# Kernel tuning notes

Measured on AMD Instinct MI355X. Metric: run time of the kernel, lower is better.

The kernel has to match this reference:

```python
import jax, jax.numpy as jnp
import numpy as np

N = 100000   # n_nodes (= ninput, identity features)
E = 1600000  # edges per adjacency (avg degree 16)
H = 128      # nhid
EPS = 1e-12


def setup_inputs() -> dict:
    key = jax.random.key(0)
    ks = jax.random.split(key, 24)
    inp = {
        'adj1_rows': jax.random.randint(ks[0], (E,), 0, N),
        'adj1_cols': jax.random.randint(ks[1], (E,), 0, N),
        'adj1_vals': jax.random.uniform(ks[2], (E,), jnp.float32) / 16.0,
        'adj2_rows': jax.random.randint(ks[3], (E,), 0, N),
        'adj2_cols': jax.random.randint(ks[4], (E,), 0, N),
        'adj2_vals': jax.random.uniform(ks[5], (E,), jnp.float32) / 16.0,
    }
    s = 1.0 / np.sqrt(H)
    inp['w1'] = jax.random.uniform(ks[6], (N, H), jnp.float32, -s, s)
    for i in range(2, 10):
        inp[f'w{i}'] = jax.random.uniform(ks[5 + i], (H, H), jnp.float32, -s, s)
    s2 = 1.0 / np.sqrt(2 * H)
    inp['m1'] = jax.random.uniform(ks[15], (H, 2 * H), jnp.float32, -s, s)
    inp['b1'] = jnp.zeros((2 * H,), jnp.float32)
    inp['m2'] = jax.random.uniform(ks[16], (2 * H, 2 * H), jnp.float32, -s2, s2)
    inp['b2'] = jnp.zeros((2 * H,), jnp.float32)
    inp['m3'] = jax.random.uniform(ks[17], (2 * H, 1), jnp.float32, -s2, s2)
    inp['b3'] = jnp.zeros((1,), jnp.float32)
    return inp


def _spmm(rows, cols, vals, x):
    # sparse [N,N] @ dense [N,H] via gather + segment_sum
    return jax.ops.segment_sum(vals[:, None] * x[cols], rows, num_segments=N)


def _l2norm(x):
    # F.normalize(x, p=2, dim=1)
    n = jnp.sqrt(jnp.sum(x * x, axis=1, keepdims=True))
    return x / jnp.maximum(n, EPS)


def _mlp(x, m1, b1, m2, b2, m3, b3):
    # dropout inactive (eval mode) for deterministic reference
    h = jax.nn.relu(x @ m1 + b1)
    h = jax.nn.relu(h @ m2 + b2)
    return h @ m3 + b3  # [N,1]


def _branch(rows, cols, vals, w1, ws, mlp_params):
    x = jax.nn.relu(_spmm(rows, cols, vals, w1))
    x = _l2norm(x)
    score = _mlp(x, *mlp_params)
    for i, w in enumerate(ws):
        x = jax.nn.relu(_spmm(rows, cols, vals, x @ w))
        if i < len(ws) - 1:  # last layer (gc9) is relu only, no normalize
            x = _l2norm(x)
        score = score + _mlp(x, *mlp_params)
    return score


def reference(adj1_rows, adj1_cols, adj1_vals, adj2_rows, adj2_cols, adj2_vals,
              w1, w2, w3, w4, w5, w6, w7, w8, w9,
              m1, b1, m2, b2, m3, b3):
    ws = [w2, w3, w4, w5, w6, w7, w8, w9]
    mlp_params = (m1, b1, m2, b2, m3, b3)
    score1 = _branch(adj1_rows, adj1_cols, adj1_vals, w1, ws, mlp_params)
    score2 = _branch(adj2_rows, adj2_cols, adj2_vals, w1, ws, mlp_params)
    return score1 * score2  # [N,1]
```

## Files before the change

kernel.cpp:

```cpp
#include <hip/hip_runtime.h>
#include <hip/hip_fp16.h>

#define NN 100000
#define NE 1600000
#define HD 128
#define HD2 256

typedef unsigned int u32;
typedef unsigned short u16;
typedef _Float16 half8 __attribute__((ext_vector_type(8)));
typedef float floatx4 __attribute__((ext_vector_type(4)));

static inline int cdiv(int a, int b){ return (a + b - 1) / b; }

__device__ __forceinline__ u32 split_pack(float v){
  __half h;
  if(fabsf(v) < 6.103515625e-05f) h = __ushort_as_half((u16)0);
  else h = __float2half_rn(v);
  float hf = __half2float(h);
  __half l = __float2half_rn((v - hf) * 4096.0f);
  return (u32)__half_as_ushort(h) | ((u32)__half_as_ushort(l) << 16);
}

__global__ void k_zero_int(int* __restrict__ p, int n){
  int i = blockIdx.x * 256 + threadIdx.x;
  if(i < n) p[i] = 0;
}

__global__ void k_zero_f(float* __restrict__ p, int n){
  int i = blockIdx.x * 256 + threadIdx.x;
  if(i < n) p[i] = 0.f;
}

__global__ void k_hist2(const int* __restrict__ r0, const int* __restrict__ r1,
                        int* __restrict__ cnt){
  int e = blockIdx.x * 256 + threadIdx.x;
  if(e < NE){
    const int* rows = blockIdx.y ? r1 : r0;
    atomicAdd(&cnt[blockIdx.y * NN + rows[e]], 1);
  }
}

__global__ void k_scan1b(const int* __restrict__ cnt, int* __restrict__ p0,
                         int* __restrict__ p1, int* __restrict__ sums, int n){
  __shared__ int sh[256];
  int z = blockIdx.y;
  const int* c = cnt + z * n;
  int* part = z ? p1 : p0;
  int* sm = sums + z * 128;
  int tid = threadIdx.x;
  int base = blockIdx.x * 1024 + tid * 4;
  int v0 = (base + 0 < n) ? c[base + 0] : 0;
  int v1 = (base + 1 < n) ? c[base + 1] : 0;
  int v2 = (base + 2 < n) ? c[base + 2] : 0;
  int v3 = (base + 3 < n) ? c[base + 3] : 0;
  int s = v0 + v1 + v2 + v3;
  sh[tid] = s;
  __syncthreads();
  for(int d = 1; d < 256; d <<= 1){
    int t = (tid >= d) ? sh[tid - d] : 0;
    __syncthreads();
    sh[tid] += t;
    __syncthreads();
  }
  int excl = sh[tid] - s;
  if(tid == 255) sm[blockIdx.x] = sh[255];
  if(base + 0 < n) part[base + 0] = excl;
  if(base + 1 < n) part[base + 1] = excl + v0;
  if(base + 2 < n) part[base + 2] = excl + v0 + v1;
  if(base + 3 < n) part[base + 3] = excl + v0 + v1 + v2;
}

__global__ void k_scan2b(int* __restrict__ sums, int nb){
  __shared__ int sh[128];
  int* s = sums + blockIdx.x * 128;
  int tid = threadIdx.x;
  int v = (tid < nb) ? s[tid] : 0;
  sh[tid] = v;
  __syncthreads();
  for(int d = 1; d < 128; d <<= 1){
    int t = (tid >= d) ? sh[tid - d] : 0;
    __syncthreads();
    sh[tid] += t;
    __syncthreads();
  }
  if(tid < nb) s[tid] = sh[tid] - v;
}

__global__ void k_scan3b(int* __restrict__ r0, int* __restrict__ r1,
                         int* __restrict__ cursor, const int* __restrict__ sums, int n){
  int z = blockIdx.y;
  int* rowptr = z ? r1 : r0;
  int* cur = cursor + z * n;
  int off = sums[z * 128 + blockIdx.x];
  int tid = threadIdx.x;
  int base = blockIdx.x * 1024 + tid * 4;
  #pragma unroll
  for(int j = 0; j < 4; j++){
    int idx = base + j;
    if(idx < n){ int r = rowptr[idx] + off; rowptr[idx] = r; cur[idx] = r; }
  }
  if(blockIdx.x == 0 && tid == 0) rowptr[n] = NE;
}

__global__ void k_scatter2(const int* __restrict__ r0, const int* __restrict__ c0,
                           const float* __restrict__ v0,
                           const int* __restrict__ r1, const int* __restrict__ c1,
                           const float* __restrict__ v1,
                           int* __restrict__ cursor,
                           uint2* __restrict__ e0, uint2* __restrict__ e1){
  int e = blockIdx.x * 256 + threadIdx.x;
  if(e < NE){
    int z = blockIdx.y;
    const int* rows = z ? r1 : r0;
    const int* cols = z ? c1 : c0;
    const float* vals = z ? v1 : v0;
    int* cur = cursor + z * NN;
    uint2* ecv = z ? e1 : e0;
    int r = rows[e];
    int pp = atomicAdd(&cur[r], 1);
    ecv[pp] = make_uint2((u32)cols[e], __float_as_uint(vals[e]));
  }
}

__global__ void k_splitw(const float* __restrict__ W, u32* __restrict__ out,
                         int K, int N, int total){
  int idx = blockIdx.x * 256 + threadIdx.x;
  if(idx < total){
    int n = idx / K, k = idx - n * K;
    out[idx] = split_pack(W[(size_t)k * N + n]);
  }
}

template<bool NORM>
__global__ void k_spmm(const int* __restrict__ rowptr, const uint2* __restrict__ ecv,
                       const float* __restrict__ X, u32* __restrict__ outpk){
  int node = (blockIdx.x << 2) + (threadIdx.x >> 6);
  int lane = threadIdx.x & 63;
  if(node >= NN) return;
  int s = rowptr[node], e = rowptr[node + 1];
  float ax = 0.f, ay = 0.f, bx = 0.f, by = 0.f;
  int i = s;
  for(; i + 15 < e; i += 16){
    uint2 ee[16]; float2 xx[16];
    #pragma unroll
    for(int j = 0; j < 16; j++) ee[j] = ecv[i + j];
    #pragma unroll
    for(int j = 0; j < 16; j++) xx[j] = *(const float2*)(X + (size_t)ee[j].x * HD + lane * 2);
    #pragma unroll
    for(int j = 0; j < 16; j += 4){
      ax += __uint_as_float(ee[j].y)   * xx[j].x   + __uint_as_float(ee[j+1].y) * xx[j+1].x;
      ay += __uint_as_float(ee[j].y)   * xx[j].y   + __uint_as_float(ee[j+1].y) * xx[j+1].y;
      bx += __uint_as_float(ee[j+2].y) * xx[j+2].x + __uint_as_float(ee[j+3].y) * xx[j+3].x;
      by += __uint_as_float(ee[j+2].y) * xx[j+2].y + __uint_as_float(ee[j+3].y) * xx[j+3].y;
    }
  }
  for(; i + 3 < e; i += 4){
    uint2 f0 = ecv[i], f1 = ecv[i+1], f2 = ecv[i+2], f3 = ecv[i+3];
    float2 x0 = *(const float2*)(X + (size_t)f0.x * HD + lane * 2);
    float2 x1 = *(const float2*)(X + (size_t)f1.x * HD + lane * 2);
    float2 x2 = *(const float2*)(X + (size_t)f2.x * HD + lane * 2);
    float2 x3 = *(const float2*)(X + (size_t)f3.x * HD + lane * 2);
    ax += __uint_as_float(f0.y) * x0.x + __uint_as_float(f1.y) * x1.x;
    ay += __uint_as_float(f0.y) * x0.y + __uint_as_float(f1.y) * x1.y;
    bx += __uint_as_float(f2.y) * x2.x + __uint_as_float(f3.y) * x3.x;
    by += __uint_as_float(f2.y) * x2.y + __uint_as_float(f3.y) * x3.y;
  }
  for(; i < e; i++){
    uint2 f0 = ecv[i];
    float2 xv = *(const float2*)(X + (size_t)f0.x * HD + lane * 2);
    ax += __uint_as_float(f0.y) * xv.x;
    ay += __uint_as_float(f0.y) * xv.y;
  }
  ax += bx; ay += by;
  ax = fmaxf(ax, 0.f);
  ay = fmaxf(ay, 0.f);
  if(NORM){
    float ss = ax * ax + ay * ay;
    #pragma unroll
    for(int o = 32; o >= 1; o >>= 1) ss += __shfl_xor(ss, o, 64);
    float scale = 1.f / fmaxf(sqrtf(ss), 1e-12f);
    ax *= scale; ay *= scale;
  }
  *(uint2*)(outpk + (size_t)node * HD + lane * 2) = make_uint2(split_pack(ax), split_pack(ay));
}

template<int MODE>
__launch_bounds__(256, 2)
__global__ void k_mfma_gemm(const u32* __restrict__ Apk, const u32* __restrict__ Btpk,
                            const u32* __restrict__ Bt1pk,
                            const float* __restrict__ bias, float* __restrict__ Yout,
                            u32* __restrict__ Hout, const float* __restrict__ m3,
                            float* __restrict__ score, int M, int K, int N){
  __shared__ u16 As_h[128 * 40], As_l[128 * 40];
  __shared__ u16 Bs_h[128 * 40], Bs_l[128 * 40];
  const int tid = threadIdx.x;
  const int lane = tid & 63, wid = tid >> 6;
  const int lm = lane & 15, lg = lane >> 4;
  const int mq = (wid & 1) * 64, nq = (wid >> 1) * 64;
  const int m0 = blockIdx.x * 128;
  int n0 = blockIdx.y * 128;
  const u32* Bt = Btpk;
  bool m0path = true;
  if(MODE == 3){
    m0path = (blockIdx.y == 0);
    if(m0path){ n0 = 0; }
    else      { n0 = (blockIdx.y - 1) * 128; Bt = Bt1pk; }
  }

  floatx4 accA[4][4], accB[4][4];
  #pragma unroll
  for(int i = 0; i < 4; i++)
    #pragma unroll
    for(int j = 0; j < 4; j++){
      accA[i][j] = (floatx4){0.f, 0.f, 0.f, 0.f};
      accB[i][j] = (floatx4){0.f, 0.f, 0.f, 0.f};
    }

  for(int k0 = 0; k0 < K; k0 += 32){
    uint4 av[4], bv[4];
    #pragma unroll
    for(int j = 0; j < 4; j++){
      int li = tid + j * 256;
      int row = li >> 3, kc = (li & 7) * 4;
      int ar = m0 + row; if(ar >= M) ar = M - 1;
      av[j] = *(const uint4*)(Apk + (size_t)ar * K + k0 + kc);
      bv[j] = *(const uint4*)(Bt + (size_t)(n0 + row) * K + k0 + kc);
    }
    if(k0) __syncthreads();
    #pragma unroll
    for(int j = 0; j < 4; j++){
      int li = tid + j * 256;
      int row = li >> 3, kc = (li & 7) * 4;
      int base = row * 40 + kc;
      ushort4 h, l;
      h.x = (u16)(av[j].x & 0xffff); l.x = (u16)(av[j].x >> 16);
      h.y = (u16)(av[j].y & 0xffff); l.y = (u16)(av[j].y >> 16);
      h.z = (u16)(av[j].z & 0xffff); l.z = (u16)(av[j].z >> 16);
      h.w = (u16)(av[j].w & 0xffff); l.w = (u16)(av[j].w >> 16);
      *(ushort4*)&As_h[base] = h;
      *(ushort4*)&As_l[base] = l;
      h.x = (u16)(bv[j].x & 0xffff); l.x = (u16)(bv[j].x >> 16);
      h.y = (u16)(bv[j].y & 0xffff); l.y = (u16)(bv[j].y >> 16);
      h.z = (u16)(bv[j].z & 0xffff); l.z = (u16)(bv[j].z >> 16);
      h.w = (u16)(bv[j].w & 0xffff); l.w = (u16)(bv[j].w >> 16);
      *(ushort4*)&Bs_h[base] = h;
      *(ushort4*)&Bs_l[base] = l;
    }
    __syncthreads();

    half8 fa_h[4], fa_l[4], fb_h[4], fb_l[4];
    #pragma unroll
    for(int s = 0; s < 4; s++){
      int ra = (mq + s * 16 + lm) * 40 + lg * 8;
      fa_h[s] = *(const half8*)&As_h[ra];
      fa_l[s] = *(const half8*)&As_l[ra];
      int rb = (nq + s * 16 + lm) * 40 + lg * 8;
      fb_h[s] = *(const half8*)&Bs_h[rb];
      fb_l[s] = *(const half8*)&Bs_l[rb];
    }
    #pragma unroll
    for(int i = 0; i < 4; i++)
      #pragma unroll
      for(int j = 0; j < 4; j++){
        accA[i][j] = __builtin_amdgcn_mfma_f32_16x16x32_f16(fa_h[i], fb_h[j], accA[i][j], 0, 0, 0);
        accB[i][j] = __builtin_amdgcn_mfma_f32_16x16x32_f16(fa_h[i], fb_l[j], accB[i][j], 0, 0, 0);
        accB[i][j] = __builtin_amdgcn_mfma_f32_16x16x32_f16(fa_l[i], fb_h[j], accB[i][j], 0, 0, 0);
      }
  }

  const float inv4096 = 1.f / 4096.f;
  if(MODE == 0 || (MODE == 3 && m0path)){
    int ldy = (MODE == 3) ? HD : N;
    #pragma unroll
    for(int i = 0; i < 4; i++)
      #pragma unroll
      for(int r = 0; r < 4; r++){
        int m = m0 + mq + i * 16 + lg * 4 + r;
        if(m < M){
          #pragma unroll
          for(int j = 0; j < 4; j++){
            int c = n0 + nq + j * 16 + lm;
            Yout[(size_t)m * ldy + c] = accA[i][j][r] + accB[i][j][r] * inv4096;
          }
        }
      }
  } else if(MODE == 1 || MODE == 3){
    int ldh = (MODE == 3) ? HD2 : N;
    #pragma unroll
    for(int i = 0; i < 4; i++)
      #pragma unroll
      for(int r = 0; r < 4; r++){
        int m = m0 + mq + i * 16 + lg * 4 + r;
        if(m < M){
          #pragma unroll
          for(int j = 0; j < 4; j++){
            int c = n0 + nq + j * 16 + lm;
            float v = fmaxf(accA[i][j][r] + accB[i][j][r] * inv4096 + bias[c], 0.f);
            Hout[(size_t)m * ldh + c] = split_pack(v);
          }
        }
      }
  } else {
    #pragma unroll
    for(int i = 0; i < 4; i++)
      #pragma unroll
      for(int r = 0; r < 4; r++){
        float s = 0.f;
        #pragma unroll
        for(int j = 0; j < 4; j++){
          int c = n0 + nq + j * 16 + lm;
          float v = fmaxf(accA[i][j][r] + accB[i][j][r] * inv4096 + bias[c], 0.f);
          s = fmaf(v, m3[c], s);
        }
        s += __shfl_xor(s, 1, 64);
        s += __shfl_xor(s, 2, 64);
        s += __shfl_xor(s, 4, 64);
        s += __shfl_xor(s, 8, 64);
        int m = m0 + mq + i * 16 + lg * 4 + r;
        if(lm == 0 && m < M) atomicAdd(&score[m], s);
      }
  }
}

__global__ void k_final(const float* __restrict__ sc, const float* __restrict__ b3,
                        float* __restrict__ out){
  int i = blockIdx.x * 256 + threadIdx.x;
  if(i < NN){
    float b = 9.f * b3[0];
    out[i] = (sc[i] + b) * (sc[NN + i] + b);
  }
}

extern "C" void kernel_launch(void* const* d_in, const int* in_sizes, int n_in,
                              void* d_out, int out_size, void* d_ws, size_t ws_size,
                              hipStream_t stream){
  const int*   a1r = (const int*)d_in[0];
  const int*   a1c = (const int*)d_in[1];
  const float* a1v = (const float*)d_in[2];
  const int*   a2r = (const int*)d_in[3];
  const int*   a2c = (const int*)d_in[4];
  const float* a2v = (const float*)d_in[5];
  const float* w1  = (const float*)d_in[6];
  const float* w[8];
  for(int i = 0; i < 8; i++) w[i] = (const float*)d_in[7 + i];
  const float* m1 = (const float*)d_in[15];
  const float* b1 = (const float*)d_in[16];
  const float* m2 = (const float*)d_in[17];
  const float* b2 = (const float*)d_in[18];
  const float* m3 = (const float*)d_in[19];
  const float* b3 = (const float*)d_in[20];
  float* out = (float*)d_out;

  char* base = (char*)d_ws;
  size_t off = 0;
  auto alloc = [&](size_t bytes) -> char* {
    char* r = base + off;
    off += (bytes + 255) & ~(size_t)255;
    return r;
  };
  int*   c1ptr = (int*)  alloc((size_t)(NN + 1) * 4);
  int*   c2ptr = (int*)  alloc((size_t)(NN + 1) * 4);
  uint2* ecv1  = (uint2*)alloc((size_t)NE * 8);
  uint2* ecv2  = (uint2*)alloc((size_t)NE * 8);
  int*   cursor= (int*)  alloc((size_t)2 * NN * 4);
  int*   sums  = (int*)  alloc(1024);
  float* sc    = (float*)alloc((size_t)2 * NN * 4);
  u32*   wtpk[8];
  for(int i = 0; i < 8; i++) wtpk[i] = (u32*)alloc((size_t)HD * HD * 4);
  u32*   m1tpk = (u32*)alloc((size_t)HD2 * HD * 4);
  u32*   m2tpk = (u32*)alloc((size_t)HD2 * HD2 * 4);
  u32*   xpk   = (u32*)alloc((size_t)NN * HD * 4);
  u32*   h1pk  = (u32*)alloc((size_t)NN * HD2 * 4);
  size_t need_ded = off + (((size_t)NN * HD * 4 + 255) & ~(size_t)255);
  bool ded_y = (ws_size >= need_ded);
  float* y = ded_y ? (float*)alloc((size_t)NN * HD * 4) : (float*)h1pk;

  hipLaunchKernelGGL(k_zero_int, dim3(cdiv(2 * NN, 256)), dim3(256), 0, stream, cursor, 2 * NN);
  hipLaunchKernelGGL(k_hist2, dim3(cdiv(NE, 256), 2), dim3(256), 0, stream, a1r, a2r, cursor);
  const int SCAN_BLOCKS = cdiv(NN, 1024);
  hipLaunchKernelGGL(k_scan1b, dim3(SCAN_BLOCKS, 2), dim3(256), 0, stream, cursor, c1ptr, c2ptr, sums, NN);
  hipLaunchKernelGGL(k_scan2b, dim3(2), dim3(128), 0, stream, sums, SCAN_BLOCKS);
  hipLaunchKernelGGL(k_scan3b, dim3(SCAN_BLOCKS, 2), dim3(256), 0, stream, c1ptr, c2ptr, cursor, sums, NN);
  hipLaunchKernelGGL(k_scatter2, dim3(cdiv(NE, 256), 2), dim3(256), 0, stream,
                     a1r, a1c, a1v, a2r, a2c, a2v, cursor, ecv1, ecv2);

  auto splitw = [&](const float* W, u32* o, int K, int N){
    int total = K * N;
    hipLaunchKernelGGL(k_splitw, dim3(cdiv(total, 256)), dim3(256), 0, stream, W, o, K, N, total);
  };
  for(int i = 0; i < 8; i++) splitw(w[i], wtpk[i], HD, HD);
  splitw(m1, m1tpk, HD, HD2);
  splitw(m2, m2tpk, HD2, HD2);
  hipLaunchKernelGGL(k_zero_f, dim3(cdiv(2 * NN, 256)), dim3(256), 0, stream, sc, 2 * NN);

  const int GX = cdiv(NN, 128);
  auto mode1 = [&](){
    hipLaunchKernelGGL((k_mfma_gemm<1>), dim3(GX, 2), dim3(256), 0, stream,
                       xpk, m1tpk, (const u32*)nullptr, b1, (float*)nullptr, h1pk,
                       (const float*)nullptr, (float*)nullptr, NN, HD, HD2);
  };
  auto mode2 = [&](float* score){
    hipLaunchKernelGGL((k_mfma_gemm<2>), dim3(GX, 2), dim3(256), 0, stream,
                       h1pk, m2tpk, (const u32*)nullptr, b2, (float*)nullptr, (u32*)nullptr,
                       m3, score, NN, HD2, HD2);
  };
  auto gemm0 = [&](int i){
    hipLaunchKernelGGL((k_mfma_gemm<0>), dim3(GX, 1), dim3(256), 0, stream,
                       xpk, wtpk[i], (const u32*)nullptr, (const float*)nullptr, y, (u32*)nullptr,
                       (const float*)nullptr, (float*)nullptr, NN, HD, HD);
  };
  auto fused01 = [&](int i){
    hipLaunchKernelGGL((k_mfma_gemm<3>), dim3(GX, 3), dim3(256), 0, stream,
                       xpk, wtpk[i], m1tpk, b1, y, h1pk,
                       (const float*)nullptr, (float*)nullptr, NN, HD, 0);
  };

  for(int b = 0; b < 2; b++){
    const int* rp = b ? c2ptr : c1ptr;
    const uint2* ecv = b ? ecv2 : ecv1;
    float* score = sc + (size_t)b * NN;
    hipLaunchKernelGGL((k_spmm<true>), dim3(cdiv(NN, 4)), dim3(256), 0, stream,
                       rp, ecv, w1, xpk);
    if(ded_y){
      for(int i = 0; i < 8; i++){
        fused01(i);
        mode2(score);
        if(i < 7)
          hipLaunchKernelGGL((k_spmm<true>),  dim3(cdiv(NN, 4)), dim3(256), 0, stream,
                             rp, ecv, y, xpk);
        else
          hipLaunchKernelGGL((k_spmm<false>), dim3(cdiv(NN, 4)), dim3(256), 0, stream,
                             rp, ecv, y, xpk);
      }
      mode1();
      mode2(score);
    } else {
      mode1();
      mode2(score);
      for(int i = 0; i < 8; i++){
        gemm0(i);
        if(i < 7)
          hipLaunchKernelGGL((k_spmm<true>),  dim3(cdiv(NN, 4)), dim3(256), 0, stream,
                             rp, ecv, y, xpk);
        else
          hipLaunchKernelGGL((k_spmm<false>), dim3(cdiv(NN, 4)), dim3(256), 0, stream,
                             rp, ecv, y, xpk);
        mode1();
        mode2(score);
      }
    }
  }

  hipLaunchKernelGGL(k_final, dim3(cdiv(NN, 256)), dim3(256), 0, stream, sc, b3, out);
}
```

Measured before the change: 4.715 ms.

## Split packed hi/lo fp16 planes and use direct global-to-LDS loads in MFMA GEMM

Activation and weight buffers change from interleaved u32 hi/lo packs to separate fp16 high and low planes. The GEMM now stages the full K=128 chunk of A straight into LDS with global_load_lds, using an XOR swizzle, in place of register unpacking. B fragments are read directly from global memory with no shared-memory staging. This is meant to cut the unpack ALU work and the LDS write traffic, at the cost of a larger LDS footprint (64KB per block), which may lower occupancy, and of uncoalesced, repeated global reads for B.

```diff
diff --git a/kernel.cpp b/kernel.cpp
--- a/kernel.cpp
+++ b/kernel.cpp
@@ -20,6 +20,11 @@
   float hf = __half2float(h);
   __half l = __float2half_rn((v - hf) * 4096.0f);
   return (u32)__half_as_ushort(h) | ((u32)__half_as_ushort(l) << 16);
+}
+
+__device__ __forceinline__ void gl_lds16(const u16* g, u16* l){
+  __builtin_amdgcn_global_load_lds((const __attribute__((address_space(1))) u32*)g,
+                                   (__attribute__((address_space(3))) u32*)l, 16, 0, 0);
 }
 
 __global__ void k_zero_int(int* __restrict__ p, int n){
@@ -123,18 +128,21 @@
   }
 }
 
-__global__ void k_splitw(const float* __restrict__ W, u32* __restrict__ out,
-                         int K, int N, int total){
+__global__ void k_splitw(const float* __restrict__ W, u16* __restrict__ oh,
+                         u16* __restrict__ ol, int K, int N, int total){
   int idx = blockIdx.x * 256 + threadIdx.x;
   if(idx < total){
     int n = idx / K, k = idx - n * K;
-    out[idx] = split_pack(W[(size_t)k * N + n]);
+    u32 p = split_pack(W[(size_t)k * N + n]);
+    oh[idx] = (u16)(p & 0xffffu);
+    ol[idx] = (u16)(p >> 16);
   }
 }
 
 template<bool NORM>
 __global__ void k_spmm(const int* __restrict__ rowptr, const uint2* __restrict__ ecv,
-                       const float* __restrict__ X, u32* __restrict__ outpk){
+                       const float* __restrict__ X, u16* __restrict__ Xh,
+                       u16* __restrict__ Xl){
   int node = (blockIdx.x << 2) + (threadIdx.x >> 6);
   int lane = threadIdx.x & 63;
   if(node >= NN) return;
@@ -182,30 +190,34 @@
     float scale = 1.f / fmaxf(sqrtf(ss), 1e-12f);
     ax *= scale; ay *= scale;
   }
-  *(uint2*)(outpk + (size_t)node * HD + lane * 2) = make_uint2(split_pack(ax), split_pack(ay));
+  u32 p0 = split_pack(ax), p1 = split_pack(ay);
+  *(u32*)(Xh + (size_t)node * HD + lane * 2) = (p0 & 0xffffu) | ((p1 & 0xffffu) << 16);
+  *(u32*)(Xl + (size_t)node * HD + lane * 2) = (p0 >> 16) | (p1 & 0xffff0000u);
 }
 
 template<int MODE>
 __launch_bounds__(256, 2)
-__global__ void k_mfma_gemm(const u32* __restrict__ Apk, const u32* __restrict__ Btpk,
-                            const u32* __restrict__ Bt1pk,
+__global__ void k_mfma_gemm(const u16* __restrict__ Ah, const u16* __restrict__ Al,
+                            const u16* __restrict__ Bh, const u16* __restrict__ Bl,
+                            const u16* __restrict__ B1h, const u16* __restrict__ B1l,
                             const float* __restrict__ bias, float* __restrict__ Yout,
-                            u32* __restrict__ Hout, const float* __restrict__ m3,
-                            float* __restrict__ score, int M, int K, int N){
-  __shared__ u16 As_h[128 * 40], As_l[128 * 40];
-  __shared__ u16 Bs_h[128 * 40], Bs_l[128 * 40];
+                            u16* __restrict__ Hh, u16* __restrict__ Hl,
+                            const float* __restrict__ m3, float* __restrict__ score,
+                            int M, int K, int N){
+  __shared__ u16 As_h[128 * 128];
+  __shared__ u16 As_l[128 * 128];
   const int tid = threadIdx.x;
   const int lane = tid & 63, wid = tid >> 6;
   const int lm = lane & 15, lg = lane >> 4;
   const int mq = (wid & 1) * 64, nq = (wid >> 1) * 64;
   const int m0 = blockIdx.x * 128;
   int n0 = blockIdx.y * 128;
-  const u32* Bt = Btpk;
+  const u16* Bth = Bh; const u16* Btl = Bl;
   bool m0path = true;
   if(MODE == 3){
     m0path = (blockIdx.y == 0);
     if(m0path){ n0 = 0; }
-    else      { n0 = (blockIdx.y - 1) * 128; Bt = Bt1pk; }
+    else      { n0 = (blockIdx.y - 1) * 128; Bth = B1h; Btl = B1l; }
   }
 
   floatx4 accA[4][4], accB[4][4];
@@ -217,56 +229,43 @@
       accB[i][j] = (floatx4){0.f, 0.f, 0.f, 0.f};
     }
 
-  for(int k0 = 0; k0 < K; k0 += 32){
-    uint4 av[4], bv[4];
-    #pragma unroll
-    for(int j = 0; j < 4; j++){
+  for(int kc = 0; kc < K; kc += 128){
+    if(kc) __syncthreads();
+    #pragma unroll
+    for(int j = 0; j < 8; j++){
       int li = tid + j * 256;
-      int row = li >> 3, kc = (li & 7) * 4;
+      int row = li >> 4, slot = li & 15;
+      int g = slot ^ (row & 15);
       int ar = m0 + row; if(ar >= M) ar = M - 1;
-      av[j] = *(const uint4*)(Apk + (size_t)ar * K + k0 + kc);
-      bv[j] = *(const uint4*)(Bt + (size_t)(n0 + row) * K + k0 + kc);
-    }
-    if(k0) __syncthreads();
-    #pragma unroll
-    for(int j = 0; j < 4; j++){
-      int li = tid + j * 256;
-      int row = li >> 3, kc = (li & 7) * 4;
-      int base = row * 40 + kc;
-      ushort4 h, l;
-      h.x = (u16)(av[j].x & 0xffff); l.x = (u16)(av[j].x >> 16);
-      h.y = (u16)(av[j].y & 0xffff); l.y = (u16)(av[j].y >> 16);
-      h.z = (u16)(av[j].z & 0xffff); l.z = (u16)(av[j].z >> 16);
-      h.w = (u16)(av[j].w & 0xffff); l.w = (u16)(av[j].w >> 16);
-      *(ushort4*)&As_h[base] = h;
-      *(ushort4*)&As_l[base] = l;
-      h.x = (u16)(bv[j].x & 0xffff); l.x = (u16)(bv[j].x >> 16);
-      h.y = (u16)(bv[j].y & 0xffff); l.y = (u16)(bv[j].y >> 16);
-      h.z = (u16)(bv[j].z & 0xffff); l.z = (u16)(bv[j].z >> 16);
-      h.w = (u16)(bv[j].w & 0xffff); l.w = (u16)(bv[j].w >> 16);
-      *(ushort4*)&Bs_h[base] = h;
-      *(ushort4*)&Bs_l[base] = l;
+      size_t so = (size_t)ar * K + kc + g * 8;
+      gl_lds16(Ah + so, &As_h[li * 8]);
+      gl_lds16(Al + so, &As_l[li * 8]);
     }
     __syncthreads();
-
-    half8 fa_h[4], fa_l[4], fb_h[4], fb_l[4];
-    #pragma unroll
-    for(int s = 0; s < 4; s++){
-      int ra = (mq + s * 16 + lm) * 40 + lg * 8;
-      fa_h[s] = *(const half8*)&As_h[ra];
-      fa_l[s] = *(const half8*)&As_l[ra];
-      int rb = (nq + s * 16 + lm) * 40 + lg * 8;
-      fb_h[s] = *(const half8*)&Bs_h[rb];
-      fb_l[s] = *(const half8*)&Bs_l[rb];
+    #pragma unroll
+    for(int ks = 0; ks < 4; ks++){
+      half8 fa_h[4], fa_l[4], fb_h[4], fb_l[4];
+      #pragma unroll
+      for(int s = 0; s < 4; s++){
+        int col = n0 + nq + s * 16 + lm;
+        size_t bo = (size_t)col * K + kc + ks * 32 + lg * 8;
+        fb_h[s] = *(const half8*)(Bth + bo);
+        fb_l[s] = *(const half8*)(Btl + bo);
+        int rowt = mq + s * 16 + lm;
+        int sl = (ks * 4 + lg) ^ (rowt & 15);
+        int ai = rowt * 128 + sl * 8;
+        fa_h[s] = *(const half8*)&As_h[ai];
+        fa_l[s] = *(const half8*)&As_l[ai];
+      }
+      #pragma unroll
+      for(int i = 0; i < 4; i++)
+        #pragma unroll
+        for(int j = 0; j < 4; j++){
+          accA[i][j] = __builtin_amdgcn_mfma_f32_16x16x32_f16(fa_h[i], fb_h[j], accA[i][j], 0, 0, 0);
+          accB[i][j] = __builtin_amdgcn_mfma_f32_16x16x32_f16(fa_h[i], fb_l[j], accB[i][j], 0, 0, 0);
+          accB[i][j] = __builtin_amdgcn_mfma_f32_16x16x32_f16(fa_l[i], fb_h[j], accB[i][j], 0, 0, 0);
+        }
     }
-    #pragma unroll
-    for(int i = 0; i < 4; i++)
-      #pragma unroll
-      for(int j = 0; j < 4; j++){
-        accA[i][j] = __builtin_amdgcn_mfma_f32_16x16x32_f16(fa_h[i], fb_h[j], accA[i][j], 0, 0, 0);
-        accB[i][j] = __builtin_amdgcn_mfma_f32_16x16x32_f16(fa_h[i], fb_l[j], accB[i][j], 0, 0, 0);
-        accB[i][j] = __builtin_amdgcn_mfma_f32_16x16x32_f16(fa_l[i], fb_h[j], accB[i][j], 0, 0, 0);
-      }
   }
 
   const float inv4096 = 1.f / 4096.f;
@@ -286,7 +285,6 @@
         }
       }
   } else if(MODE == 1 || MODE == 3){
-    int ldh = (MODE == 3) ? HD2 : N;
     #pragma unroll
     for(int i = 0; i < 4; i++)
       #pragma unroll
@@ -297,7 +295,9 @@
           for(int j = 0; j < 4; j++){
             int c = n0 + nq + j * 16 + lm;
             float v = fmaxf(accA[i][j][r] + accB[i][j][r] * inv4096 + bias[c], 0.f);
-            Hout[(size_t)m * ldh + c] = split_pack(v);
+            u32 p = split_pack(v);
+            Hh[(size_t)m * HD2 + c] = (u16)(p & 0xffffu);
+            Hl[(size_t)m * HD2 + c] = (u16)(p >> 16);
           }
         }
       }
@@ -366,15 +366,22 @@
   int*   cursor= (int*)  alloc((size_t)2 * NN * 4);
   int*   sums  = (int*)  alloc(1024);
   float* sc    = (float*)alloc((size_t)2 * NN * 4);
-  u32*   wtpk[8];
-  for(int i = 0; i < 8; i++) wtpk[i] = (u32*)alloc((size_t)HD * HD * 4);
-  u32*   m1tpk = (u32*)alloc((size_t)HD2 * HD * 4);
-  u32*   m2tpk = (u32*)alloc((size_t)HD2 * HD2 * 4);
-  u32*   xpk   = (u32*)alloc((size_t)NN * HD * 4);
-  u32*   h1pk  = (u32*)alloc((size_t)NN * HD2 * 4);
+  u16*   wth[8]; u16* wtl[8];
+  for(int i = 0; i < 8; i++){
+    wth[i] = (u16*)alloc((size_t)HD * HD * 2);
+    wtl[i] = (u16*)alloc((size_t)HD * HD * 2);
+  }
+  u16*   m1h = (u16*)alloc((size_t)HD2 * HD * 2);
+  u16*   m1l = (u16*)alloc((size_t)HD2 * HD * 2);
+  u16*   m2h = (u16*)alloc((size_t)HD2 * HD2 * 2);
+  u16*   m2l = (u16*)alloc((size_t)HD2 * HD2 * 2);
+  u16*   Xh  = (u16*)alloc((size_t)NN * HD * 2);
+  u16*   Xl  = (u16*)alloc((size_t)NN * HD * 2);
+  u16*   H1h = (u16*)alloc((size_t)NN * HD2 * 2);
+  u16*   H1l = (u16*)alloc((size_t)NN * HD2 * 2);
   size_t need_ded = off + (((size_t)NN * HD * 4 + 255) & ~(size_t)255);
   bool ded_y = (ws_size >= need_ded);
-  float* y = ded_y ? (float*)alloc((size_t)NN * HD * 4) : (float*)h1pk;
+  float* y = ded_y ? (float*)alloc((size_t)NN * HD * 4) : (float*)H1h;
 
   hipLaunchKernelGGL(k_zero_int, dim3(cdiv(2 * NN, 256)), dim3(256), 0, stream, cursor, 2 * NN);
   hipLaunchKernelGGL(k_hist2, dim3(cdiv(NE, 256), 2), dim3(256), 0, stream, a1r, a2r, cursor);
@@ -385,34 +392,38 @@
   hipLaunchKernelGGL(k_scatter2, dim3(cdiv(NE, 256), 2), dim3(256), 0, stream,
                      a1r, a1c, a1v, a2r, a2c, a2v, cursor, ecv1, ecv2);
 
-  auto splitw = [&](const float* W, u32* o, int K, int N){
+  auto splitw = [&](const float* W, u16* oh, u16* ol, int K, int N){
     int total = K * N;
-    hipLaunchKernelGGL(k_splitw, dim3(cdiv(total, 256)), dim3(256), 0, stream, W, o, K, N, total);
-  };
-  for(int i = 0; i < 8; i++) splitw(w[i], wtpk[i], HD, HD);
-  splitw(m1, m1tpk, HD, HD2);
-  splitw(m2, m2tpk, HD2, HD2);
+    hipLaunchKernelGGL(k_splitw, dim3(cdiv(total, 256)), dim3(256), 0, stream, W, oh, ol, K, N, total);
+  };
+  for(int i = 0; i < 8; i++) splitw(w[i], wth[i], wtl[i], HD, HD);
+  splitw(m1, m1h, m1l, HD, HD2);
+  splitw(m2, m2h, m2l, HD2, HD2);
   hipLaunchKernelGGL(k_zero_f, dim3(cdiv(2 * NN, 256)), dim3(256), 0, stream, sc, 2 * NN);
 
   const int GX = cdiv(NN, 128);
   auto mode1 = [&](){
     hipLaunchKernelGGL((k_mfma_gemm<1>), dim3(GX, 2), dim3(256), 0, stream,
-                       xpk, m1tpk, (const u32*)nullptr, b1, (float*)nullptr, h1pk,
+                       Xh, Xl, m1h, m1l, (const u16*)nullptr, (const u16*)nullptr,
+                       b1, (float*)nullptr, H1h, H1l,
                        (const float*)nullptr, (float*)nullptr, NN, HD, HD2);
   };
   auto mode2 = [&](float* score){
     hipLaunchKernelGGL((k_mfma_gemm<2>), dim3(GX, 2), dim3(256), 0, stream,
-                       h1pk, m2tpk, (const u32*)nullptr, b2, (float*)nullptr, (u32*)nullptr,
+                       H1h, H1l, m2h, m2l, (const u16*)nullptr, (const u16*)nullptr,
+                       b2, (float*)nullptr, (u16*)nullptr, (u16*)nullptr,
                        m3, score, NN, HD2, HD2);
   };
   auto gemm0 = [&](int i){
     hipLaunchKernelGGL((k_mfma_gemm<0>), dim3(GX, 1), dim3(256), 0, stream,
-                       xpk, wtpk[i], (const u32*)nullptr, (const float*)nullptr, y, (u32*)nullptr,
+                       Xh, Xl, wth[i], wtl[i], (const u16*)nullptr, (const u16*)nullptr,
+                       (const float*)nullptr, y, (u16*)nullptr, (u16*)nullptr,
                        (const float*)nullptr, (float*)nullptr, NN, HD, HD);
   };
   auto fused01 = [&](int i){
     hipLaunchKernelGGL((k_mfma_gemm<3>), dim3(GX, 3), dim3(256), 0, stream,
-                       xpk, wtpk[i], m1tpk, b1, y, h1pk,
+                       Xh, Xl, wth[i], wtl[i], m1h, m1l,
+                       b1, y, H1h, H1l,
                        (const float*)nullptr, (float*)nullptr, NN, HD, 0);
   };
 
@@ -421,17 +432,17 @@
     const uint2* ecv = b ? ecv2 : ecv1;
     float* score = sc + (size_t)b * NN;
     hipLaunchKernelGGL((k_spmm<true>), dim3(cdiv(NN, 4)), dim3(256), 0, stream,
-                       rp, ecv, w1, xpk);
+                       rp, ecv, w1, Xh, Xl);
     if(ded_y){
       for(int i = 0; i < 8; i++){
         fused01(i);
         mode2(score);
         if(i < 7)
           hipLaunchKernelGGL((k_spmm<true>),  dim3(cdiv(NN, 4)), dim3(256), 0, stream,
-                             rp, ecv, y, xpk);
+                             rp, ecv, y, Xh, Xl);
         else
           hipLaunchKernelGGL((k_spmm<false>), dim3(cdiv(NN, 4)), dim3(256), 0, stream,
-                             rp, ecv, y, xpk);
+                             rp, ecv, y, Xh, Xl);
       }
       mode1();
       mode2(score);
@@ -442,10 +453,10 @@
         gemm0(i);
         if(i < 7)
           hipLaunchKernelGGL((k_spmm<true>),  dim3(cdiv(NN, 4)), dim3(256), 0, stream,
-                             rp, ecv, y, xpk);
+                             rp, ecv, y, Xh, Xl);
         else
           hipLaunchKernelGGL((k_spmm<false>), dim3(cdiv(NN, 4)), dim3(256), 0, stream,
-                             rp, ecv, y, xpk);
+                             rp, ecv, y, Xh, Xl);
         mode1();
         mode2(score);
       }
```

Result: slower. 7.598 ms (+61.2%).

## Replace atomic COO-to-CSR scatter with two-pass bucketed binning scatter

Applied to the files above, without the earlier changes.

The single-pass scatter, which did one global atomicAdd per edge into random rows, is replaced by two passes. The first pass bins each 4096-edge chunk in LDS by coarse row bucket (196 rows per bucket) and writes the chunk out in contiguous runs. The second pass places each bucket's edges into their rows using LDS atomics. This targets global atomic contention and scattered uncoalesced writes during CSR construction, at the cost of an extra round trip of edge data through a temporary buffer held in h1pk scratch. The CSR build is a one-time setup step next to many SpMM and GEMM layers, so the effect on total time may be small.

```diff
diff --git a/kernel.cpp b/kernel.cpp
--- a/kernel.cpp
+++ b/kernel.cpp
@@ -5,6 +5,10 @@
 #define NE 1600000
 #define HD 128
 #define HD2 256
+
+#define NBK 512
+#define RPB 196
+#define CH  4096
 
 typedef unsigned int u32;
 typedef unsigned short u16;
@@ -103,23 +107,113 @@
   if(blockIdx.x == 0 && tid == 0) rowptr[n] = NE;
 }
 
-__global__ void k_scatter2(const int* __restrict__ r0, const int* __restrict__ c0,
-                           const float* __restrict__ v0,
-                           const int* __restrict__ r1, const int* __restrict__ c1,
-                           const float* __restrict__ v1,
-                           int* __restrict__ cursor,
-                           uint2* __restrict__ e0, uint2* __restrict__ e1){
-  int e = blockIdx.x * 256 + threadIdx.x;
-  if(e < NE){
-    int z = blockIdx.y;
-    const int* rows = z ? r1 : r0;
-    const int* cols = z ? c1 : c0;
-    const float* vals = z ? v1 : v0;
-    int* cur = cursor + z * NN;
-    uint2* ecv = z ? e1 : e0;
-    int r = rows[e];
-    int pp = atomicAdd(&cur[r], 1);
-    ecv[pp] = make_uint2((u32)cols[e], __float_as_uint(vals[e]));
+__global__ void k_init_bcur(const int* __restrict__ c1ptr, const int* __restrict__ c2ptr,
+                            int* __restrict__ cursor){
+  int b = blockIdx.x * 256 + threadIdx.x;
+  int z = blockIdx.y;
+  if(b < NBK){
+    const int* rp = z ? c2ptr : c1ptr;
+    int r = b * RPB; if(r > NN) r = NN;
+    cursor[z * NN + b] = rp[r];
+  }
+}
+
+__global__ void k_binscatter(const int* __restrict__ r0a, const int* __restrict__ c0a,
+                             const float* __restrict__ v0a,
+                             const int* __restrict__ r1a, const int* __restrict__ c1a,
+                             const float* __restrict__ v1a,
+                             int* __restrict__ bcur,
+                             u32* __restrict__ sr0, uint2* __restrict__ sv0,
+                             u32* __restrict__ sr1, uint2* __restrict__ sv1){
+  __shared__ int cnt[NBK];
+  __shared__ int bstart[NBK];
+  __shared__ int gbase[NBK];
+  __shared__ int sh[256];
+  __shared__ u32 srow[CH];
+  __shared__ uint2 scvs[CH];
+  int z = blockIdx.y;
+  const int* rows = z ? r1a : r0a;
+  const int* cols = z ? c1a : c0a;
+  const float* vals = z ? v1a : v0a;
+  int* cur = bcur + z * NN;
+  u32* osr = z ? sr1 : sr0;
+  uint2* osv = z ? sv1 : sv0;
+  int t = threadIdx.x;
+  for(int i = t; i < NBK; i += 256) cnt[i] = 0;
+  __syncthreads();
+  int e0 = blockIdx.x * CH;
+  int total = NE - e0; if(total > CH) total = CH;
+  int r_[16], c_[16], b_[16], k_[16]; float v_[16];
+  #pragma unroll
+  for(int k = 0; k < 16; k++){
+    int e = e0 + t + k * 256;
+    b_[k] = -1;
+    if(e < NE){
+      r_[k] = rows[e]; c_[k] = cols[e]; v_[k] = vals[e];
+      b_[k] = r_[k] / RPB;
+      k_[k] = atomicAdd(&cnt[b_[k]], 1);
+    }
+  }
+  __syncthreads();
+  int v0 = cnt[2 * t], v1 = cnt[2 * t + 1];
+  int s2 = v0 + v1;
+  sh[t] = s2;
+  __syncthreads();
+  for(int d = 1; d < 256; d <<= 1){
+    int tv = (t >= d) ? sh[t - d] : 0;
+    __syncthreads();
+    sh[t] += tv;
+    __syncthreads();
+  }
+  int excl = sh[t] - s2;
+  bstart[2 * t] = excl;
+  bstart[2 * t + 1] = excl + v0;
+  __syncthreads();
+  #pragma unroll
+  for(int k = 0; k < 16; k++){
+    if(b_[k] >= 0){
+      int slot = bstart[b_[k]] + k_[k];
+      srow[slot] = (u32)r_[k];
+      scvs[slot] = make_uint2((u32)c_[k], __float_as_uint(v_[k]));
+    }
+  }
+  for(int b = t; b < NBK; b += 256){
+    int c = cnt[b];
+    if(c > 0) gbase[b] = atomicAdd(&cur[b], c);
+  }
+  __syncthreads();
+  for(int i = t; i < total; i += 256){
+    u32 r = srow[i];
+    int b = (int)r / RPB;
+    int dest = gbase[b] + (i - bstart[b]);
+    osr[dest] = r;
+    osv[dest] = scvs[i];
+  }
+}
+
+__global__ void k_bucket_place(const int* __restrict__ c1ptr, const int* __restrict__ c2ptr,
+                               const u32* __restrict__ sr0, const uint2* __restrict__ sv0,
+                               const u32* __restrict__ sr1, const uint2* __restrict__ sv1,
+                               uint2* __restrict__ e0, uint2* __restrict__ e1){
+  __shared__ int cur[RPB];
+  int z = blockIdx.y;
+  const int* rp = z ? c2ptr : c1ptr;
+  const u32* sr = z ? sr1 : sr0;
+  const uint2* sv = z ? sv1 : sv0;
+  uint2* ecv = z ? e1 : e0;
+  int b = blockIdx.x;
+  int r0 = b * RPB;
+  if(r0 >= NN) return;
+  int rend = r0 + RPB; if(rend > NN) rend = NN;
+  int t = threadIdx.x;
+  for(int r = t; r < rend - r0; r += 256) cur[r] = rp[r0 + r];
+  __syncthreads();
+  int s = rp[r0], e = rp[rend];
+  for(int i = s + t; i < e; i += 256){
+    u32 r = sr[i];
+    uint2 cv = sv[i];
+    int p = atomicAdd(&cur[r - r0], 1);
+    ecv[p] = cv;
   }
 }
 
@@ -376,14 +470,23 @@
   bool ded_y = (ws_size >= need_ded);
   float* y = ded_y ? (float*)alloc((size_t)NN * HD * 4) : (float*)h1pk;
 
+  char* hb = (char*)h1pk;
+  uint2* sv1 = (uint2*)hb;
+  u32*   sr1 = (u32*)(hb + (size_t)NE * 8);
+  uint2* sv2 = (uint2*)(hb + (size_t)NE * 12);
+  u32*   sr2 = (u32*)(hb + (size_t)NE * 20);
+
   hipLaunchKernelGGL(k_zero_int, dim3(cdiv(2 * NN, 256)), dim3(256), 0, stream, cursor, 2 * NN);
   hipLaunchKernelGGL(k_hist2, dim3(cdiv(NE, 256), 2), dim3(256), 0, stream, a1r, a2r, cursor);
   const int SCAN_BLOCKS = cdiv(NN, 1024);
   hipLaunchKernelGGL(k_scan1b, dim3(SCAN_BLOCKS, 2), dim3(256), 0, stream, cursor, c1ptr, c2ptr, sums, NN);
   hipLaunchKernelGGL(k_scan2b, dim3(2), dim3(128), 0, stream, sums, SCAN_BLOCKS);
   hipLaunchKernelGGL(k_scan3b, dim3(SCAN_BLOCKS, 2), dim3(256), 0, stream, c1ptr, c2ptr, cursor, sums, NN);
-  hipLaunchKernelGGL(k_scatter2, dim3(cdiv(NE, 256), 2), dim3(256), 0, stream,
-                     a1r, a1c, a1v, a2r, a2c, a2v, cursor, ecv1, ecv2);
+  hipLaunchKernelGGL(k_init_bcur, dim3(cdiv(NBK, 256), 2), dim3(256), 0, stream, c1ptr, c2ptr, cursor);
+  hipLaunchKernelGGL(k_binscatter, dim3(cdiv(NE, CH), 2), dim3(256), 0, stream,
+                     a1r, a1c, a1v, a2r, a2c, a2v, cursor, sr1, sv1, sr2, sv2);
+  hipLaunchKernelGGL(k_bucket_place, dim3(NBK, 2), dim3(256), 0, stream,
+                     c1ptr, c2ptr, sr1, sv1, sr2, sv2, ecv1, ecv2);
 
   auto splitw = [&](const float* W, u32* o, int K, int N){
     int total = K * N;
```

After: 4.553 ms. 1.04x faster.
